# Kernel tuning notes

Hardware: AMD Instinct MI355X
Metric: run time of the kernel (lower is better)

## Reference

```python
import jax, jax.numpy as jnp
import numpy as np

ROPE_BASE = 10000.0
WINDOW = 1024  # per_layer_sliding_window
SCALE = 0.08838834764831845  # 1/sqrt(128)
NEG_INF = -1e30


def _apply_rope(x, positions):
    # x: [B, S, H, D]; positions: [B, S] int
    D = x.shape[-1]
    inv_freq = 1.0 / (ROPE_BASE ** (jnp.arange(0, D, 2, dtype=jnp.float32) / D))  # [D/2]
    ang = positions.astype(jnp.float32)[..., None] * inv_freq          # [B, S, D/2]
    cos = jnp.cos(ang)[:, :, None, :]                                   # [B, S, 1, D/2]
    sin = jnp.sin(ang)[:, :, None, :]
    x1, x2 = x[..., : D // 2], x[..., D // 2 :]
    return jnp.concatenate([x1 * cos - x2 * sin, x2 * cos + x1 * sin], axis=-1)


def setup_inputs() -> dict:
    key = jax.random.key(0)
    k1, k2, k3, k4 = jax.random.split(key, 4)
    B, S, H, KV, D = 1, 2048, 32, 8, 128
    q = jax.random.normal(k1, (B, S, H, D), dtype=jnp.float32)
    k = jax.random.normal(k2, (B, S, KV, D), dtype=jnp.float32)
    v = jax.random.normal(k3, (B, S, KV, D), dtype=jnp.float32)
    positions = jnp.broadcast_to(jnp.arange(S, dtype=jnp.int32), (B, S))
    sinks = jax.random.normal(k4, (H,), dtype=jnp.float32)
    return {"q": q, "k": k, "v": v, "positions": positions, "sinks": sinks}


def reference(q, k, v, positions, sinks):
    # q: [B,S,H,D]; k,v: [B,S,KV,D]; positions: [B,S]; sinks: [H]
    B, S, H, D = q.shape
    KV = k.shape[2]
    group = H // KV

    qr = _apply_rope(q, positions)
    kr = _apply_rope(k, positions)

    # GQA: expand kv heads to match q heads
    kr = jnp.repeat(kr, group, axis=2)  # [B,S,H,D]
    ve = jnp.repeat(v, group, axis=2)   # [B,S,H,D]

    scores = jnp.einsum("bqhd,bkhd->bhqk", qr, kr) * SCALE  # [B,H,Q,K]

    pq = positions[:, :, None]  # [B,Q,1]
    pk = positions[:, None, :]  # [B,1,K]
    allowed = (pk <= pq) & (pq - pk < WINDOW)               # causal + sliding window
    scores = jnp.where(allowed[:, None, :, :], scores, NEG_INF)

    # softmax with per-head attention sink logit in the denominator
    sink = sinks[None, :, None]                             # [1,H,1]
    m = jnp.maximum(jnp.max(scores, axis=-1), sink)         # [B,H,Q]
    p = jnp.exp(scores - m[..., None])                      # [B,H,Q,K]
    denom = jnp.sum(p, axis=-1) + jnp.exp(sink - m)         # [B,H,Q]
    out = jnp.einsum("bhqk,bkhd->bqhd", p, ve) / denom.transpose(0, 2, 1)[..., None]
    return out  # [B,S,H,D]
```

## Files before the change

kernel.cpp:

```cpp
#include <hip/hip_runtime.h>

#define S_LEN 2048
#define NH 32
#define NKV 8
#define HD 128
#define WINDOW 1024
#define NEG_INF_F -1e30f
#define NEG_L2_10K_O64 -0.2076205059304601f
#define LOG2E_F 1.442695040888963f

typedef unsigned short ushort_t;
typedef __attribute__((ext_vector_type(8))) short short8;
typedef __attribute__((ext_vector_type(4))) float floatx4;
typedef __attribute__((ext_vector_type(16))) float floatx16;
typedef __attribute__((ext_vector_type(4))) int intx4;

static __device__ __forceinline__ float fexp2(float x) {
  return __builtin_amdgcn_exp2f(x);
}

static __device__ __forceinline__ ushort_t f2bf(float f) {
  union { float f; unsigned u; } un; un.f = f;
  unsigned r = un.u + 0x7fffu + ((un.u >> 16) & 1u);
  return (ushort_t)(r >> 16);
}

static __device__ __forceinline__ unsigned pack2bf(float a, float b) {
  return (unsigned)f2bf(a) | ((unsigned)f2bf(b) << 16);
}

static __device__ __forceinline__ unsigned packP(float a, float b) {
  unsigned ua = __builtin_bit_cast(unsigned, a) + 0x8000u;
  unsigned ub = __builtin_bit_cast(unsigned, b) + 0x8000u;
  return __builtin_amdgcn_perm(ub, ua, 0x07060302u);
}

__device__ __forceinline__ void gl_lds16(const ushort_t* g, ushort_t* l) {
  __builtin_amdgcn_global_load_lds(
      (const __attribute__((address_space(1))) unsigned int*)g,
      (__attribute__((address_space(3))) unsigned int*)l, 16, 0, 0);
}

__global__ __launch_bounds__(256) void prep_kv(
    const float* __restrict__ k, const float* __restrict__ v,
    const int* __restrict__ positions, ushort_t* __restrict__ Kr,
    ushort_t* __restrict__ Vt) {
  __shared__ float lv[64][129];
  const int kv = blockIdx.x & 7;
  const int s0 = (blockIdx.x >> 3) * 64;
  const int tid = threadIdx.x;
  {
    const int i = tid & 63;
    const int wrow = tid >> 6;
    const float invf = fexp2((float)i * NEG_L2_10K_O64);
#pragma unroll 4
    for (int it = 0; it < 16; ++it) {
      int s = s0 + it * 4 + wrow;
      float pos = (float)positions[s];
      const float* kp = k + ((size_t)s * NKV + kv) * HD;
      float x1 = kp[i], x2 = kp[i + 64];
      float sn, cs;
      __sincosf(pos * invf, &sn, &cs);
      ushort_t* o = Kr + ((size_t)kv * S_LEN + s) * HD;
      o[i] = f2bf(x1 * cs - x2 * sn);
      o[i + 64] = f2bf(x2 * cs + x1 * sn);
    }
  }
  {
    const int d = tid & 127;
    const int r2 = tid >> 7;
#pragma unroll
    for (int it = 0; it < 32; ++it) {
      int row = it * 2 + r2;
      lv[row][d] = v[((size_t)(s0 + row) * NKV + kv) * HD + d];
    }
  }
  __syncthreads();
  {
    unsigned* Vreg = (unsigned*)(Vt + ((size_t)(kv * 32 + (s0 >> 6)) * HD) * 64);
#pragma unroll
    for (int it = 0; it < 16; ++it) {
      int idx = it * 256 + tid;
      int d = idx >> 5, j = idx & 31;
      Vreg[idx] = pack2bf(lv[2 * j][d], lv[2 * j + 1][d]);
    }
  }
}

__global__ __launch_bounds__(256, 3) void attn_kernel(
    const float* __restrict__ q, const int* __restrict__ positions,
    const float* __restrict__ sinks, const ushort_t* __restrict__ Kr,
    const ushort_t* __restrict__ Vt, float* __restrict__ out) {
  __shared__ __align__(16) ushort_t smem[16384];
  __shared__ float lsx[64];

  const int tid = threadIdx.x;
  const int w = tid >> 6;
  const int lane = tid & 63;
  const int quad = lane >> 4;
  const int l16 = lane & 15;
  const int hp = w >> 1;
  const int kh = w & 1;
  const int kv = blockIdx.x & 7;
  const int bid = blockIdx.x >> 3;
  const int h0 = kv * 4 + hp * 2;
  const float QSCALE = (float)(0.08838834764831845 * 1.4426950408889634);

  const ushort_t* KrH = Kr + (size_t)kv * S_LEN * HD;
  const ushort_t* VtH = Vt + (size_t)kv * 32 * HD * 64;

  int tiles[2];
  int ntiles;
  if (bid < 64) { tiles[0] = bid + 64; tiles[1] = 0; ntiles = 1; }
  else          { tiles[0] = bid - 64; tiles[1] = 127 - bid; ntiles = 2; }

  int kgo0, kgo1, vgo0, vgo1;
  { int key = tid >> 4;          kgo0 = key * HD + (((tid & 15) ^ (key & 15)) * 8); }
  { int s2 = 256 + tid; int key = s2 >> 4;
                                 kgo1 = key * HD + (((s2 & 15) ^ (key & 15)) * 8); }
  { int d = tid >> 2;            vgo0 = d * 64 + (((tid & 3) ^ ((d ^ (d >> 2)) & 3)) * 8); }
  { int d = 64 + (tid >> 2);     vgo1 = d * 64 + (((tid & 3) ^ ((d ^ (d >> 2)) & 3)) * 8); }
  const int kdst0 = (tid & 192) * 8;
  const int kdst1 = (256 + (tid & 192)) * 8;
  const int vdst0 = 8192 + (tid & 192) * 8;
  const int vdst1 = 8192 + 2048 + (tid & 192) * 8;
  const int vroff = ((2 * kh + (lane >> 5)) ^ ((lane ^ (lane >> 2)) & 3)) * 8;

  auto stage = [&](int b, int koff) {
    const ushort_t* kb = KrH + (size_t)koff * HD;
    const ushort_t* vb = VtH + (size_t)(koff >> 6) * HD * 64 + (koff & 32);
    gl_lds16(kb + kgo0, smem + b * 4096 + kdst0);
    gl_lds16(kb + kgo1, smem + b * 4096 + kdst1);
    gl_lds16(vb + vgo0, smem + b * 4096 + vdst0);
    gl_lds16(vb + vgo1, smem + b * 4096 + vdst1);
  };

  for (int ti = 0; ti < ntiles; ++ti) {
    const int tile = tiles[ti];
    const int q0 = tile * 16;

    {
      const int hw = kv * 4 + w;
      ushort_t* Qsw = smem + w * 2048;
      const float invf = fexp2((float)lane * NEG_L2_10K_O64);
#pragma unroll 4
      for (int row = 0; row < 16; ++row) {
        float pos = (float)positions[q0 + row];
        const float* qp = q + ((size_t)(q0 + row) * NH + hw) * HD;
        float x1 = qp[lane], x2 = qp[lane + 64];
        float sn, cs;
        __sincosf(pos * invf, &sn, &cs);
        float o1 = (x1 * cs - x2 * sn) * QSCALE;
        float o2 = (x2 * cs + x1 * sn) * QSCALE;
        int c1_ = (lane >> 3) ^ row;
        int c2_ = ((lane >> 3) + 8) ^ row;
        Qsw[row * 128 + c1_ * 8 + (lane & 7)] = f2bf(o1);
        Qsw[row * 128 + c2_ * 8 + (lane & 7)] = f2bf(o2);
      }
    }
    __syncthreads();
    short8 qf0[4], qf1[4];
    {
      const ushort_t* Qr0 = smem + (hp * 2) * 2048;
      const ushort_t* Qr1 = smem + (hp * 2 + 1) * 2048;
#pragma unroll
      for (int t = 0; t < 4; ++t) {
        int off = l16 * 128 + (((4 * t + quad) ^ l16) * 8);
        qf0[t] = *(const short8*)&Qr0[off];
        qf1[t] = *(const short8*)&Qr1[off];
      }
    }
    __syncthreads();

    floatx16 O[4];
#pragma unroll
    for (int i = 0; i < 4; ++i)
#pragma unroll
      for (int e = 0; e < 16; ++e) O[i][e] = 0.f;
    float lsumA = 0.f, lsumB = 0.f;

    const int cbeg = (q0 > 1023) ? ((q0 - 1023) >> 5) : 0;
    const int cend = (q0 + 15) >> 5;

    stage(0, cbeg * 32);
    __syncthreads();

    for (int ci = cbeg; ci <= cend; ++ci) {
      const int b = (ci - cbeg) & 1;
      const int koff = ci * 32;
      if (ci < cend) stage(b ^ 1, koff + 32);

      const ushort_t* KsB = smem + b * 4096 + (kh * 16) * 128;
      floatx4 sA = {0.f, 0.f, 0.f, 0.f}, sB = {0.f, 0.f, 0.f, 0.f};
#pragma unroll
      for (int t = 0; t < 4; ++t) {
        short8 kf = *(const short8*)&KsB[l16 * 128 + (((4 * t + quad) ^ l16) * 8)];
        sA = __builtin_amdgcn_mfma_f32_16x16x32_bf16(kf, qf0[t], sA, 0, 0, 0);
        sB = __builtin_amdgcn_mfma_f32_16x16x32_bf16(kf, qf1[t], sB, 0, 0, 0);
      }

      if (koff + 31 > q0 || koff < q0 - 1008) {
        const int qp_ = q0 + l16;
        const int kb_ = koff + kh * 16 + quad * 4;
#pragma unroll
        for (int r = 0; r < 4; ++r) {
          int ki = kb_ + r;
          bool ok = (ki <= qp_) && (qp_ - ki < WINDOW);
          if (!ok) { sA[r] = NEG_INF_F; sB[r] = NEG_INF_F; }
        }
      }

      float pA[4], pB[4];
#pragma unroll
      for (int r = 0; r < 4; ++r) { pA[r] = fexp2(sA[r]); pB[r] = fexp2(sB[r]); }
      lsumA += (pA[0] + pA[1]) + (pA[2] + pA[3]);
      lsumB += (pB[0] + pB[1]) + (pB[2] + pB[3]);

      unsigned a01 = packP(pA[0], pA[1]), a23 = packP(pA[2], pA[3]);
      unsigned b01 = packP(pB[0], pB[1]), b23 = packP(pB[2], pB[3]);
      intx4 bi;
      {
        const int s0l = (quad >> 1) * 32 + l16;
        int xa0 = __shfl((int)a01, s0l),      xa1 = __shfl((int)a23, s0l);
        int xa2 = __shfl((int)a01, s0l + 16), xa3 = __shfl((int)a23, s0l + 16);
        int yb0 = __shfl((int)b01, s0l),      yb1 = __shfl((int)b23, s0l);
        int yb2 = __shfl((int)b01, s0l + 16), yb3 = __shfl((int)b23, s0l + 16);
        const bool hb = (quad & 1);
        bi[0] = hb ? yb0 : xa0; bi[1] = hb ? yb1 : xa1;
        bi[2] = hb ? yb2 : xa2; bi[3] = hb ? yb3 : xa3;
      }
      short8 pf = __builtin_bit_cast(short8, bi);

      const ushort_t* VsB = smem + 8192 + b * 4096;
#pragma unroll
      for (int tl = 0; tl < 4; ++tl) {
        short8 vf = *(const short8*)&VsB[(tl * 32 + (lane & 31)) * 32 + vroff];
        O[tl] = __builtin_amdgcn_mfma_f32_32x32x16_bf16(vf, pf, O[tl], 0, 0, 0);
      }

      __syncthreads();
    }

    lsumA += __shfl_xor(lsumA, 16); lsumA += __shfl_xor(lsumA, 32);
    lsumB += __shfl_xor(lsumB, 16); lsumB += __shfl_xor(lsumB, 32);
    float* Lf = (float*)smem;
    const int lfb = hp * 2048 + lane * 4;
    float rl = 0.f;

    if (kh == 1) {
      if (quad == 0) {
        lsx[hp * 32 + l16] = lsumA;
        lsx[hp * 32 + 16 + l16] = lsumB;
      }
#pragma unroll
      for (int u = 0; u < 2; ++u)
#pragma unroll
        for (int r4 = 0; r4 < 4; ++r4)
          *(floatx4*)&Lf[lfb + (u * 4 + r4) * 256] =
              (floatx4){O[u][r4 * 4], O[u][r4 * 4 + 1], O[u][r4 * 4 + 2], O[u][r4 * 4 + 3]};
    }
    __syncthreads();
    if (kh == 0) {
      float denA = lsumA + lsx[hp * 32 + l16] + fexp2(sinks[h0] * LOG2E_F);
      float denB = lsumB + lsx[hp * 32 + 16 + l16] + fexp2(sinks[h0 + 1] * LOG2E_F);
      rl = (quad & 1) ? (1.0f / denB) : (1.0f / denA);
      float* op = out + ((size_t)(q0 + l16) * NH + (h0 + (quad & 1))) * HD;
#pragma unroll
      for (int u = 0; u < 2; ++u)
#pragma unroll
        for (int r4 = 0; r4 < 4; ++r4) {
          floatx4 pv = *(const floatx4*)&Lf[lfb + (u * 4 + r4) * 256];
          floatx4 vv;
#pragma unroll
          for (int e = 0; e < 4; ++e) vv[e] = (O[u][r4 * 4 + e] + pv[e]) * rl;
          *(floatx4*)(op + u * 32 + r4 * 8 + (quad >> 1) * 4) = vv;
        }
    }
    __syncthreads();
    if (kh == 1) {
#pragma unroll
      for (int u = 0; u < 2; ++u)
#pragma unroll
        for (int r4 = 0; r4 < 4; ++r4)
          *(floatx4*)&Lf[lfb + (u * 4 + r4) * 256] =
              (floatx4){O[u + 2][r4 * 4], O[u + 2][r4 * 4 + 1],
                        O[u + 2][r4 * 4 + 2], O[u + 2][r4 * 4 + 3]};
    }
    __syncthreads();
    if (kh == 0) {
      float* op = out + ((size_t)(q0 + l16) * NH + (h0 + (quad & 1))) * HD;
#pragma unroll
      for (int u = 0; u < 2; ++u)
#pragma unroll
        for (int r4 = 0; r4 < 4; ++r4) {
          floatx4 pv = *(const floatx4*)&Lf[lfb + (u * 4 + r4) * 256];
          floatx4 vv;
#pragma unroll
          for (int e = 0; e < 4; ++e) vv[e] = (O[u + 2][r4 * 4 + e] + pv[e]) * rl;
          *(floatx4*)(op + (u + 2) * 32 + r4 * 8 + (quad >> 1) * 4) = vv;
        }
    }
    __syncthreads();
  }
}

extern "C" void kernel_launch(void* const* d_in, const int* in_sizes, int n_in,
                              void* d_out, int out_size, void* d_ws, size_t ws_size,
                              hipStream_t stream) {
  const float* q = (const float*)d_in[0];
  const float* k = (const float*)d_in[1];
  const float* v = (const float*)d_in[2];
  const int* positions = (const int*)d_in[3];
  const float* sinks = (const float*)d_in[4];
  float* out = (float*)d_out;

  ushort_t* Kr = (ushort_t*)d_ws;
  ushort_t* Vt = Kr + (size_t)NKV * S_LEN * HD;

  prep_kv<<<NKV * (S_LEN / 64), 256, 0, stream>>>(k, v, positions, Kr, Vt);
  attn_kernel<<<NKV * 96, 256, 0, stream>>>(q, positions, sinks, Kr, Vt, out);
}
```

Baseline: 138.7 us.

## Use 16x16x16 MFMA for PV so P feeds B operand without shuffles

Replaces the 32x32x16 bf16 MFMA for the P·V product with 16x16x16 bf16 MFMAs, one per head and 16-wide slice of the head dimension. This lets each lane's packed P values serve directly as the B operand, removing the eight cross-lane shuffles and selects per key chunk. The V LDS swizzle and read offsets are rewritten to match the new fragment layout, and the epilogue is restructured for the new accumulator layout. In exchange it issues twice as many smaller MFMAs and eight V fragment reads per chunk instead of four.

```diff
diff --git a/kernel.cpp b/kernel.cpp
--- a/kernel.cpp
+++ b/kernel.cpp
@@ -10,10 +10,10 @@
 #define LOG2E_F 1.442695040888963f
 
 typedef unsigned short ushort_t;
+typedef __attribute__((ext_vector_type(4))) short bf16x4;
 typedef __attribute__((ext_vector_type(8))) short short8;
+typedef __attribute__((ext_vector_type(2))) unsigned uint2v;
 typedef __attribute__((ext_vector_type(4))) float floatx4;
-typedef __attribute__((ext_vector_type(16))) float floatx16;
-typedef __attribute__((ext_vector_type(4))) int intx4;
 
 static __device__ __forceinline__ float fexp2(float x) {
   return __builtin_amdgcn_exp2f(x);
@@ -118,13 +118,14 @@
   { int key = tid >> 4;          kgo0 = key * HD + (((tid & 15) ^ (key & 15)) * 8); }
   { int s2 = 256 + tid; int key = s2 >> 4;
                                  kgo1 = key * HD + (((s2 & 15) ^ (key & 15)) * 8); }
-  { int d = tid >> 2;            vgo0 = d * 64 + (((tid & 3) ^ ((d ^ (d >> 2)) & 3)) * 8); }
-  { int d = 64 + (tid >> 2);     vgo1 = d * 64 + (((tid & 3) ^ ((d ^ (d >> 2)) & 3)) * 8); }
+  { int n = tid;       int d = n >> 2; vgo0 = d * 64 + (((n & 3) ^ (d & 3)) * 8); }
+  { int n = 256 + tid; int d = n >> 2; vgo1 = d * 64 + (((n & 3) ^ (d & 3)) * 8); }
   const int kdst0 = (tid & 192) * 8;
   const int kdst1 = (256 + (tid & 192)) * 8;
   const int vdst0 = 8192 + (tid & 192) * 8;
   const int vdst1 = 8192 + 2048 + (tid & 192) * 8;
-  const int vroff = ((2 * kh + (lane >> 5)) ^ ((lane ^ (lane >> 2)) & 3)) * 8;
+  const int kb8 = kh * 2 + (quad >> 1);
+  const int vrd = (l16 * 4 + (kb8 ^ (l16 & 3))) * 8 + (quad & 1) * 4;
 
   auto stage = [&](int b, int koff) {
     const ushort_t* kb = KrH + (size_t)koff * HD;
@@ -172,11 +173,12 @@
     }
     __syncthreads();
 
-    floatx16 O[4];
-#pragma unroll
-    for (int i = 0; i < 4; ++i)
-#pragma unroll
-      for (int e = 0; e < 16; ++e) O[i][e] = 0.f;
+    floatx4 OA[8], OB[8];
+#pragma unroll
+    for (int i = 0; i < 8; ++i) {
+      OA[i] = (floatx4){0.f, 0.f, 0.f, 0.f};
+      OB[i] = (floatx4){0.f, 0.f, 0.f, 0.f};
+    }
     float lsumA = 0.f, lsumB = 0.f;
 
     const int cbeg = (q0 > 1023) ? ((q0 - 1023) >> 5) : 0;
@@ -216,26 +218,18 @@
       lsumA += (pA[0] + pA[1]) + (pA[2] + pA[3]);
       lsumB += (pB[0] + pB[1]) + (pB[2] + pB[3]);
 
-      unsigned a01 = packP(pA[0], pA[1]), a23 = packP(pA[2], pA[3]);
-      unsigned b01 = packP(pB[0], pB[1]), b23 = packP(pB[2], pB[3]);
-      intx4 bi;
-      {
-        const int s0l = (quad >> 1) * 32 + l16;
-        int xa0 = __shfl((int)a01, s0l),      xa1 = __shfl((int)a23, s0l);
-        int xa2 = __shfl((int)a01, s0l + 16), xa3 = __shfl((int)a23, s0l + 16);
-        int yb0 = __shfl((int)b01, s0l),      yb1 = __shfl((int)b23, s0l);
-        int yb2 = __shfl((int)b01, s0l + 16), yb3 = __shfl((int)b23, s0l + 16);
-        const bool hb = (quad & 1);
-        bi[0] = hb ? yb0 : xa0; bi[1] = hb ? yb1 : xa1;
-        bi[2] = hb ? yb2 : xa2; bi[3] = hb ? yb3 : xa3;
-      }
-      short8 pf = __builtin_bit_cast(short8, bi);
+      uint2v ua, ub;
+      ua[0] = packP(pA[0], pA[1]); ua[1] = packP(pA[2], pA[3]);
+      ub[0] = packP(pB[0], pB[1]); ub[1] = packP(pB[2], pB[3]);
+      bf16x4 pfA = __builtin_bit_cast(bf16x4, ua);
+      bf16x4 pfB = __builtin_bit_cast(bf16x4, ub);
 
       const ushort_t* VsB = smem + 8192 + b * 4096;
 #pragma unroll
-      for (int tl = 0; tl < 4; ++tl) {
-        short8 vf = *(const short8*)&VsB[(tl * 32 + (lane & 31)) * 32 + vroff];
-        O[tl] = __builtin_amdgcn_mfma_f32_32x32x16_bf16(vf, pf, O[tl], 0, 0, 0);
+      for (int dt = 0; dt < 8; ++dt) {
+        bf16x4 vf = *(const bf16x4*)&VsB[vrd + dt * 512];
+        OA[dt] = __builtin_amdgcn_mfma_f32_16x16x16bf16_1k(vf, pfA, OA[dt], 0, 0, 0);
+        OB[dt] = __builtin_amdgcn_mfma_f32_16x16x16bf16_1k(vf, pfB, OB[dt], 0, 0, 0);
       }
 
       __syncthreads();
@@ -244,63 +238,47 @@
     lsumA += __shfl_xor(lsumA, 16); lsumA += __shfl_xor(lsumA, 32);
     lsumB += __shfl_xor(lsumB, 16); lsumB += __shfl_xor(lsumB, 32);
     float* Lf = (float*)smem;
-    const int lfb = hp * 2048 + lane * 4;
-    float rl = 0.f;
-
-    if (kh == 1) {
-      if (quad == 0) {
-        lsx[hp * 32 + l16] = lsumA;
-        lsx[hp * 32 + 16 + l16] = lsumB;
-      }
-#pragma unroll
-      for (int u = 0; u < 2; ++u)
-#pragma unroll
-        for (int r4 = 0; r4 < 4; ++r4)
-          *(floatx4*)&Lf[lfb + (u * 4 + r4) * 256] =
-              (floatx4){O[u][r4 * 4], O[u][r4 * 4 + 1], O[u][r4 * 4 + 2], O[u][r4 * 4 + 3]};
-    }
-    __syncthreads();
-    if (kh == 0) {
-      float denA = lsumA + lsx[hp * 32 + l16] + fexp2(sinks[h0] * LOG2E_F);
-      float denB = lsumB + lsx[hp * 32 + 16 + l16] + fexp2(sinks[h0 + 1] * LOG2E_F);
-      rl = (quad & 1) ? (1.0f / denB) : (1.0f / denA);
-      float* op = out + ((size_t)(q0 + l16) * NH + (h0 + (quad & 1))) * HD;
-#pragma unroll
-      for (int u = 0; u < 2; ++u)
-#pragma unroll
-        for (int r4 = 0; r4 < 4; ++r4) {
-          floatx4 pv = *(const floatx4*)&Lf[lfb + (u * 4 + r4) * 256];
+    const int lfb = lane * 4;
+    float rlA = 0.f, rlB = 0.f;
+
+    if (kh == 1 && quad == 0) {
+      lsx[hp * 32 + l16] = lsumA;
+      lsx[hp * 32 + 16 + l16] = lsumB;
+    }
+#pragma unroll
+    for (int m = 0; m < 2; ++m) {
+      if (kh == 1) {
+#pragma unroll
+        for (int t = 0; t < 4; ++t) {
+          *(floatx4*)&Lf[((hp * 2 + 0) * 4 + t) * 256 + lfb] = OA[m * 4 + t];
+          *(floatx4*)&Lf[((hp * 2 + 1) * 4 + t) * 256 + lfb] = OB[m * 4 + t];
+        }
+      }
+      __syncthreads();
+      if (kh == 0) {
+        if (m == 0) {
+          float denA = lsumA + lsx[hp * 32 + l16] + fexp2(sinks[h0] * LOG2E_F);
+          float denB = lsumB + lsx[hp * 32 + 16 + l16] + fexp2(sinks[h0 + 1] * LOG2E_F);
+          rlA = 1.0f / denA;
+          rlB = 1.0f / denB;
+        }
+        float* opA = out + ((size_t)(q0 + l16) * NH + h0) * HD + quad * 4;
+        float* opB = opA + HD;
+#pragma unroll
+        for (int t = 0; t < 4; ++t) {
+          floatx4 pv = *(const floatx4*)&Lf[((hp * 2 + 0) * 4 + t) * 256 + lfb];
           floatx4 vv;
 #pragma unroll
-          for (int e = 0; e < 4; ++e) vv[e] = (O[u][r4 * 4 + e] + pv[e]) * rl;
-          *(floatx4*)(op + u * 32 + r4 * 8 + (quad >> 1) * 4) = vv;
+          for (int e = 0; e < 4; ++e) vv[e] = (OA[m * 4 + t][e] + pv[e]) * rlA;
+          *(floatx4*)(opA + (m * 4 + t) * 16) = vv;
+          pv = *(const floatx4*)&Lf[((hp * 2 + 1) * 4 + t) * 256 + lfb];
+#pragma unroll
+          for (int e = 0; e < 4; ++e) vv[e] = (OB[m * 4 + t][e] + pv[e]) * rlB;
+          *(floatx4*)(opB + (m * 4 + t) * 16) = vv;
         }
-    }
-    __syncthreads();
-    if (kh == 1) {
-#pragma unroll
-      for (int u = 0; u < 2; ++u)
-#pragma unroll
-        for (int r4 = 0; r4 < 4; ++r4)
-          *(floatx4*)&Lf[lfb + (u * 4 + r4) * 256] =
-              (floatx4){O[u + 2][r4 * 4], O[u + 2][r4 * 4 + 1],
-                        O[u + 2][r4 * 4 + 2], O[u + 2][r4 * 4 + 3]};
-    }
-    __syncthreads();
-    if (kh == 0) {
-      float* op = out + ((size_t)(q0 + l16) * NH + (h0 + (quad & 1))) * HD;
-#pragma unroll
-      for (int u = 0; u < 2; ++u)
-#pragma unroll
-        for (int r4 = 0; r4 < 4; ++r4) {
-          floatx4 pv = *(const floatx4*)&Lf[lfb + (u * 4 + r4) * 256];
-          floatx4 vv;
-#pragma unroll
-          for (int e = 0; e < 4; ++e) vv[e] = (O[u + 2][r4 * 4 + e] + pv[e]) * rl;
-          *(floatx4*)(op + (u + 2) * 32 + r4 * 8 + (quad >> 1) * 4) = vv;
-        }
-    }
-    __syncthreads();
+      }
+      __syncthreads();
+    }
   }
 }
 
```

Measured after the change: 140.6 us. About the same (+1.4%).
